# Kernel tuning notes

Hardware: AMD Instinct MI355X
Metric: run time of the kernel (lower is better)

Reference implementation:

```python
import jax, jax.numpy as jnp
import numpy as np

DIM, NH, NL, NP, HD, FF = 256, 8, 4, 4, 32, 1024
LN_EPS = 1e-5


def _ln(x, w, b):
    m = jnp.mean(x, axis=-1, keepdims=True)
    v = jnp.mean((x - m) ** 2, axis=-1, keepdims=True)
    return (x - m) * jax.lax.rsqrt(v + LN_EPS) * w + b


def _sample_level(value_l, loc, H, W):
    # value_l: (B, H*W, nH, hd) ; loc: (B, Lq, nH, P, 2) normalized coords in [0,1]
    B, Lq, nH, P, _ = loc.shape
    # grid_sample(align_corners=False): pixel coord = norm * size - 0.5
    x = loc[..., 0] * W - 0.5
    y = loc[..., 1] * H - 0.5
    x0 = jnp.floor(x)
    y0 = jnp.floor(y)
    wx1 = x - x0
    wy1 = y - y0
    wx0 = 1.0 - wx1
    wy0 = 1.0 - wy1
    x0i = x0.astype(jnp.int32)
    y0i = y0.astype(jnp.int32)

    def corner(xi, yi, w):
        valid = ((xi >= 0) & (xi < W) & (yi >= 0) & (yi < H)).astype(value_l.dtype)
        idx = jnp.clip(yi, 0, H - 1) * W + jnp.clip(xi, 0, W - 1)
        idx = idx.transpose(0, 1, 3, 2).reshape(B, Lq * P, nH, 1)  # per-head gather index
        v = jnp.take_along_axis(value_l, idx, axis=1).reshape(B, Lq, P, nH, -1)
        wm = (w * valid).transpose(0, 1, 3, 2)[..., None]  # (B,Lq,P,nH,1)
        return v * wm

    return (corner(x0i, y0i, wx0 * wy0) + corner(x0i + 1, y0i, wx1 * wy0)
            + corner(x0i, y0i + 1, wx0 * wy1) + corner(x0i + 1, y0i + 1, wx1 * wy1))


def _msdeform_attn(q, value, ref, shapes_np, starts_np, W_off, b_off, W_attn, b_attn):
    B, S, _ = q.shape
    off = (q @ W_off + b_off).reshape(B, S, NH, NL, NP, 2)
    attn = jax.nn.softmax((q @ W_attn + b_attn).reshape(B, S, NH, NL * NP), axis=-1)
    attn = attn.reshape(B, S, NH, NL, NP)
    # offset normalizer is (W, H) per level
    norm = jnp.asarray(shapes_np[:, ::-1].copy(), dtype=q.dtype)  # (NL, 2)
    loc = ref[:, :, None, :, None, :] + off / norm[None, None, None, :, None, :]
    outs = []
    for l in range(NL):
        H, W = int(shapes_np[l, 0]), int(shapes_np[l, 1])
        s = int(starts_np[l])
        vl = value[:, s:s + H * W]  # (B, H*W, NH, HD)
        outs.append(_sample_level(vl, loc[:, :, :, l], H, W))  # (B,S,P,NH,HD)
    samp = jnp.stack(outs, axis=2)  # (B,S,NL,P,NH,HD)
    w = attn.transpose(0, 1, 3, 4, 2)[..., None]  # (B,S,NL,P,NH,1)
    return (samp * w).sum(axis=(2, 3)).reshape(B, S, NH * HD)


def setup_inputs() -> dict:
    key = jax.random.key(0)
    ks = jax.random.split(key, 16)
    shapes = np.array([[64, 64], [32, 32], [16, 16], [8, 8]], dtype=np.int64)
    starts = np.array([0, 4096, 5120, 5376], dtype=np.int64)
    B, S = 4, 5440
    std = 0.02
    return {
        "input": jax.random.normal(ks[0], (B, S, DIM), jnp.float32),
        "pos": jax.random.normal(ks[1], (B, S, DIM), jnp.float32),
        "reference_point": jax.random.uniform(ks[2], (B, S, NL, 2), jnp.float32),
        "shape": shapes,
        "level_start": starts,
        "ln1_w": jnp.ones((DIM,), jnp.float32),
        "ln1_b": jnp.zeros((DIM,), jnp.float32),
        "W_off": jax.random.normal(ks[3], (DIM, NH * NL * NP * 2), jnp.float32) * std,
        "b_off": jax.random.normal(ks[4], (NH * NL * NP * 2,), jnp.float32) * 0.1,
        "W_attn": jax.random.normal(ks[5], (DIM, NH * NL * NP), jnp.float32) * std,
        "b_attn": jnp.zeros((NH * NL * NP,), jnp.float32),
        "W_val": jax.random.normal(ks[6], (DIM, DIM), jnp.float32) * std,
        "b_val": jnp.zeros((DIM,), jnp.float32),
        "W_out": jax.random.normal(ks[7], (DIM, DIM), jnp.float32) * std,
        "b_out": jnp.zeros((DIM,), jnp.float32),
        "ln2_w": jnp.ones((DIM,), jnp.float32),
        "ln2_b": jnp.zeros((DIM,), jnp.float32),
        "ff_w1": jax.random.normal(ks[8], (DIM, FF), jnp.float32) * std,
        "ff_b1": jnp.zeros((FF,), jnp.float32),
        "ff_w2": jax.random.normal(ks[9], (FF, DIM), jnp.float32) * std,
        "ff_b2": jnp.zeros((DIM,), jnp.float32),
    }


def reference(input, pos, reference_point, shape, level_start,
              ln1_w, ln1_b, W_off, b_off, W_attn, b_attn, W_val, b_val,
              W_out, b_out, ln2_w, ln2_b, ff_w1, ff_b1, ff_w2, ff_b2):
    shapes_np = np.asarray(shape)
    starts_np = np.asarray(level_start)
    B, S, _ = input.shape
    # pre-norm query with positional embedding
    q = _ln(input, ln1_w, ln1_b) + pos
    # value projection acts on the raw residual stream (input_flatten)
    value = (input @ W_val + b_val).reshape(B, S, NH, HD)
    attn_out = _msdeform_attn(q, value, reference_point, shapes_np, starts_np,
                              W_off, b_off, W_attn, b_attn) @ W_out + b_out
    x = input + attn_out  # dropout is identity in eval
    y = _ln(x, ln2_w, ln2_b)
    ff = jax.nn.relu(y @ ff_w1 + ff_b1) @ ff_w2 + ff_b2
    return x + ff
```

## Files before the change

### kernel.cpp

```cpp
#include <hip/hip_runtime.h>
#include <math.h>

#define DIM 256
#define NHEAD 8
#define NLVL 4
#define NPT 4
#define HDIM 32
#define FFDIM 1024
#define BATCH 4
#define SEQ 5440
#define MTOK (BATCH * SEQ)

typedef __attribute__((ext_vector_type(8))) short short8;
typedef __attribute__((ext_vector_type(4))) float f32x4;

__device__ __forceinline__ unsigned short f2bf(float f) {
    union { float f; unsigned int u; } x; x.f = f;
    unsigned int r = x.u + 0x7fffu + ((x.u >> 16) & 1u);
    return (unsigned short)(r >> 16);
}
__device__ __forceinline__ float bf_lo(unsigned int u) {
    union { unsigned int u; float f; } x; x.u = u << 16;
    return x.f;
}
__device__ __forceinline__ float bf_hi(unsigned int u) {
    union { unsigned int u; float f; } x; x.u = u & 0xffff0000u;
    return x.f;
}

__global__ __launch_bounds__(256) void wtprep_kernel(
    const float* __restrict__ W_val, const float* __restrict__ W_off,
    const float* __restrict__ W_attn, const float* __restrict__ W_out,
    const float* __restrict__ ff_w1, const float* __restrict__ ff_w2,
    unsigned short* __restrict__ wts)
{
    int idx = blockIdx.x * 256 + threadIdx.x;
    const float* W; int K, N, base;
    if      (idx < 65536)  { W = W_val;  K = 256;  N = 256;  base = 0; }
    else if (idx < 131072) { W = W_off;  K = 256;  N = 256;  base = 65536; }
    else if (idx < 163840) { W = W_attn; K = 256;  N = 128;  base = 131072; }
    else if (idx < 229376) { W = W_out;  K = 256;  N = 256;  base = 163840; }
    else if (idx < 491520) { W = ff_w1;  K = 256;  N = 1024; base = 229376; }
    else if (idx < 753664) { W = ff_w2;  K = 1024; N = 256;  base = 491520; }
    else return;
    int li = idx - base;
    int k = li % K;
    int n = li / K;
    wts[idx] = f2bf(W[(size_t)k * N + n]);
}

template<int COPY_BF16>
__global__ __launch_bounds__(256) void ln_kernel(
    const float* __restrict__ x, const float* __restrict__ w,
    const float* __restrict__ bvec, const float* __restrict__ addend,
    unsigned short* __restrict__ out, unsigned short* __restrict__ xbf)
{
    int wv = threadIdx.x >> 6, lane = threadIdx.x & 63;
    int token = blockIdx.x * 4 + wv;
    size_t base = (size_t)token * DIM + lane * 4;
    float4 v = *(const float4*)(x + base);
    float s  = v.x + v.y + v.z + v.w;
    float s2 = v.x * v.x + v.y * v.y + v.z * v.z + v.w * v.w;
    #pragma unroll
    for (int o = 1; o < 64; o <<= 1) {
        s  += __shfl_xor(s, o);
        s2 += __shfl_xor(s2, o);
    }
    float m  = s * (1.0f / DIM);
    float rs = rsqrtf(s2 * (1.0f / DIM) - m * m + 1e-5f);
    float4 w4 = *(const float4*)(w + lane * 4);
    float4 b4 = *(const float4*)(bvec + lane * 4);
    float4 r;
    r.x = (v.x - m) * rs * w4.x + b4.x;
    r.y = (v.y - m) * rs * w4.y + b4.y;
    r.z = (v.z - m) * rs * w4.z + b4.z;
    r.w = (v.w - m) * rs * w4.w + b4.w;
    if (addend) {
        float4 a = *(const float4*)(addend + base);
        r.x += a.x; r.y += a.y; r.z += a.z; r.w += a.w;
    }
    ushort4 o4;
    o4.x = f2bf(r.x); o4.y = f2bf(r.y); o4.z = f2bf(r.z); o4.w = f2bf(r.w);
    *(ushort4*)(out + base) = o4;
    if (COPY_BF16) {
        ushort4 c;
        c.x = f2bf(v.x); c.y = f2bf(v.y); c.z = f2bf(v.z); c.w = f2bf(v.w);
        *(ushort4*)(xbf + base) = c;
    }
}

#define LDSTR 40

template<int OUT_BF16, int RELU, int HAS_RES>
__global__ __launch_bounds__(256) void mfma_gemm(
    const unsigned short* __restrict__ A,
    const unsigned short* __restrict__ Bt,
    const float* __restrict__ bias,
    const float* __restrict__ res,
    void* __restrict__ Cout,
    int M, int N, int K)
{
    __shared__ __align__(16) unsigned short As[128 * LDSTR];
    __shared__ __align__(16) unsigned short Bs[128 * LDSTR];

    const int tid  = threadIdx.x;
    const int lane = tid & 63;
    const int wv   = tid >> 6;
    const int wr   = wv >> 1;
    const int wc   = wv & 1;
    const int m16  = lane & 15;
    const int quad = lane >> 4;

    const int bm0 = blockIdx.y * 128;
    const int bn0 = blockIdx.x * 128;

    const int srow = tid >> 2;
    const int scol = (tid & 3) * 8;

    f32x4 acc[4][4] = {};

    for (int k0 = 0; k0 < K; k0 += 32) {
        uint4 av0 = *(const uint4*)(A  + (size_t)(bm0 + srow)      * K + k0 + scol);
        uint4 av1 = *(const uint4*)(A  + (size_t)(bm0 + srow + 64) * K + k0 + scol);
        uint4 bv0 = *(const uint4*)(Bt + (size_t)(bn0 + srow)      * K + k0 + scol);
        uint4 bv1 = *(const uint4*)(Bt + (size_t)(bn0 + srow + 64) * K + k0 + scol);
        if (k0) __syncthreads();
        *(uint4*)&As[(srow)      * LDSTR + scol] = av0;
        *(uint4*)&As[(srow + 64) * LDSTR + scol] = av1;
        *(uint4*)&Bs[(srow)      * LDSTR + scol] = bv0;
        *(uint4*)&Bs[(srow + 64) * LDSTR + scol] = bv1;
        __syncthreads();

        short8 af[4], bf[4];
        #pragma unroll
        for (int i = 0; i < 4; i++)
            af[i] = *(const short8*)&As[(wr * 64 + i * 16 + m16) * LDSTR + quad * 8];
        #pragma unroll
        for (int j = 0; j < 4; j++)
            bf[j] = *(const short8*)&Bs[(wc * 64 + j * 16 + m16) * LDSTR + quad * 8];

        #pragma unroll
        for (int i = 0; i < 4; i++)
            #pragma unroll
            for (int j = 0; j < 4; j++)
                acc[i][j] = __builtin_amdgcn_mfma_f32_16x16x32_bf16(
                    af[i], bf[j], acc[i][j], 0, 0, 0);
    }

    #pragma unroll
    for (int i = 0; i < 4; i++) {
        #pragma unroll
        for (int j = 0; j < 4; j++) {
            int colb = bn0 + wc * 64 + j * 16 + m16;
            float bcol = bias[colb];
            #pragma unroll
            for (int r = 0; r < 4; r++) {
                int rowb = bm0 + wr * 64 + i * 16 + quad * 4 + r;
                float v = acc[i][j][r] + bcol;
                if (HAS_RES) v += res[(size_t)rowb * N + colb];
                if (RELU) v = fmaxf(v, 0.0f);
                if (OUT_BF16)
                    ((unsigned short*)Cout)[(size_t)rowb * N + colb] = f2bf(v);
                else
                    ((float*)Cout)[(size_t)rowb * N + colb] = v;
            }
        }
    }
}

__global__ __launch_bounds__(256) void msdeform_kernel(
    const unsigned short* __restrict__ value,
    const float* __restrict__ off_buf,
    const float* __restrict__ attn_buf,
    const float* __restrict__ ref,
    unsigned short* __restrict__ samp_out)
{
    const int Hs[NLVL] = {64, 32, 16, 8};
    const int Ws[NLVL] = {64, 32, 16, 8};
    const int St[NLVL] = {0, 4096, 5120, 5376};

    const int t  = threadIdx.x;
    const int tt = t >> 5;
    const int h  = (t >> 2) & 7;
    const int dg = t & 3;
    const int token = blockIdx.x * 8 + tt;
    const int b = token / SEQ;

    __shared__ float s_attn[8][NHEAD][16];
    __shared__ float s_loc[8][NHEAD][16][2];

    float4 a4 = *(const float4*)(attn_buf + (size_t)token * 128 + h * 16 + dg * 4);
    *(float4*)&s_attn[tt][h][dg * 4] = a4;

    const float* offp = off_buf + (size_t)token * 256 + h * 32 + dg * 8;
    float4 o0 = *(const float4*)(offp);
    float4 o1 = *(const float4*)(offp + 4);
    float fWd = (float)Ws[dg], fHd = (float)Hs[dg];
    float rx = ref[(size_t)token * 8 + dg * 2 + 0];
    float ry = ref[(size_t)token * 8 + dg * 2 + 1];
    s_loc[tt][h][dg * 4 + 0][0] = rx + o0.x / fWd;
    s_loc[tt][h][dg * 4 + 0][1] = ry + o0.y / fHd;
    s_loc[tt][h][dg * 4 + 1][0] = rx + o0.z / fWd;
    s_loc[tt][h][dg * 4 + 1][1] = ry + o0.w / fHd;
    s_loc[tt][h][dg * 4 + 2][0] = rx + o1.x / fWd;
    s_loc[tt][h][dg * 4 + 2][1] = ry + o1.y / fHd;
    s_loc[tt][h][dg * 4 + 3][0] = rx + o1.z / fWd;
    s_loc[tt][h][dg * 4 + 3][1] = ry + o1.w / fHd;
    __syncthreads();

    if (dg == 0) {
        float mx = -1e30f;
        #pragma unroll
        for (int i = 0; i < 16; i++) mx = fmaxf(mx, s_attn[tt][h][i]);
        float sum = 0.0f;
        #pragma unroll
        for (int i = 0; i < 16; i++) {
            float e = __expf(s_attn[tt][h][i] - mx);
            s_attn[tt][h][i] = e;
            sum += e;
        }
        float inv = 1.0f / sum;
        #pragma unroll
        for (int i = 0; i < 16; i++) s_attn[tt][h][i] *= inv;
    }
    __syncthreads();

    const size_t vbase = ((size_t)b * SEQ) * DIM + h * HDIM + dg * 8;

    float acc[8] = {};
    #pragma unroll
    for (int l = 0; l < NLVL; l++) {
        const int Hl = Hs[l], Wl = Ws[l], s0 = St[l];
        const float fW = (float)Wl, fH = (float)Hl;
        #pragma unroll
        for (int p = 0; p < NPT; p++) {
            int i = l * 4 + p;
            float aw = s_attn[tt][h][i];
            float x = s_loc[tt][h][i][0] * fW - 0.5f;
            float y = s_loc[tt][h][i][1] * fH - 0.5f;
            float x0f = floorf(x), y0f = floorf(y);
            float wx1 = x - x0f, wy1 = y - y0f;
            float wx0 = 1.0f - wx1, wy0 = 1.0f - wy1;
            int x0 = (int)x0f, y0 = (int)y0f;
            #pragma unroll
            for (int cy = 0; cy < 2; cy++) {
                int yi = y0 + cy;
                bool vy = (yi >= 0) && (yi < Hl);
                int yc = min(max(yi, 0), Hl - 1);
                float wy = cy ? wy1 : wy0;
                #pragma unroll
                for (int cx = 0; cx < 2; cx++) {
                    int xi = x0 + cx;
                    bool vx = (xi >= 0) && (xi < Wl);
                    int xc = min(max(xi, 0), Wl - 1);
                    float cw = aw * wy * (cx ? wx1 : wx0) * ((vx && vy) ? 1.0f : 0.0f);
                    uint4 v = *(const uint4*)(value + vbase + (size_t)(s0 + yc * Wl + xc) * DIM);
                    acc[0] = fmaf(cw, bf_lo(v.x), acc[0]);
                    acc[1] = fmaf(cw, bf_hi(v.x), acc[1]);
                    acc[2] = fmaf(cw, bf_lo(v.y), acc[2]);
                    acc[3] = fmaf(cw, bf_hi(v.y), acc[3]);
                    acc[4] = fmaf(cw, bf_lo(v.z), acc[4]);
                    acc[5] = fmaf(cw, bf_hi(v.z), acc[5]);
                    acc[6] = fmaf(cw, bf_lo(v.w), acc[6]);
                    acc[7] = fmaf(cw, bf_hi(v.w), acc[7]);
                }
            }
        }
    }

    uint4 o;
    o.x = (unsigned int)f2bf(acc[0]) | ((unsigned int)f2bf(acc[1]) << 16);
    o.y = (unsigned int)f2bf(acc[2]) | ((unsigned int)f2bf(acc[3]) << 16);
    o.z = (unsigned int)f2bf(acc[4]) | ((unsigned int)f2bf(acc[5]) << 16);
    o.w = (unsigned int)f2bf(acc[6]) | ((unsigned int)f2bf(acc[7]) << 16);
    *(uint4*)(samp_out + (size_t)token * DIM + h * HDIM + dg * 8) = o;
}

extern "C" void kernel_launch(void* const* d_in, const int* in_sizes, int n_in,
                              void* d_out, int out_size, void* d_ws, size_t ws_size,
                              hipStream_t stream) {
    const float* input = (const float*)d_in[0];
    const float* pos   = (const float*)d_in[1];
    const float* ref   = (const float*)d_in[2];
    const float* ln1_w = (const float*)d_in[5];
    const float* ln1_b = (const float*)d_in[6];
    const float* W_off = (const float*)d_in[7];
    const float* b_off = (const float*)d_in[8];
    const float* W_attn = (const float*)d_in[9];
    const float* b_attn = (const float*)d_in[10];
    const float* W_val = (const float*)d_in[11];
    const float* b_val = (const float*)d_in[12];
    const float* W_out = (const float*)d_in[13];
    const float* b_out = (const float*)d_in[14];
    const float* ln2_w = (const float*)d_in[15];
    const float* ln2_b = (const float*)d_in[16];
    const float* ff_w1 = (const float*)d_in[17];
    const float* ff_b1 = (const float*)d_in[18];
    const float* ff_w2 = (const float*)d_in[19];
    const float* ff_b2 = (const float*)d_in[20];
    float* out = (float*)d_out;

    const size_t M = MTOK;
    float* ws = (float*)d_ws;

    unsigned short* input_bf = (unsigned short*)(ws);
    unsigned short* y_bf     = input_bf;
    unsigned short* q_bf     = (unsigned short*)(ws + M * 128);
    unsigned short* samp_bf  = q_bf;
    float*  off_buf  = ws + M * 256;
    float*  x_buf    = off_buf;
    float*  attn_buf = ws + M * 512;
    unsigned short* val_bf   = (unsigned short*)(ws + M * 640);
    unsigned short* h_bf     = (unsigned short*)(ws + M * 512);
    unsigned short* wts      = (unsigned short*)(ws + M * 1024);

    unsigned short* wval_t  = wts;
    unsigned short* woff_t  = wval_t  + 256 * 256;
    unsigned short* wattn_t = woff_t  + 256 * 256;
    unsigned short* wout_t  = wattn_t + 128 * 256;
    unsigned short* ffw1_t  = wout_t  + 256 * 256;
    unsigned short* ffw2_t  = ffw1_t  + 1024 * 256;

    dim3 blk(256);

    wtprep_kernel<<<dim3((753664 + 255) / 256), blk, 0, stream>>>(
        W_val, W_off, W_attn, W_out, ff_w1, ff_w2, wts);

    ln_kernel<1><<<dim3(M / 4), blk, 0, stream>>>(
        input, ln1_w, ln1_b, pos, q_bf, input_bf);

    mfma_gemm<1,0,0><<<dim3(256/128, M/128), blk, 0, stream>>>(
        input_bf, wval_t, b_val, nullptr, val_bf, M, 256, 256);

    mfma_gemm<0,0,0><<<dim3(256/128, M/128), blk, 0, stream>>>(
        q_bf, woff_t, b_off, nullptr, off_buf, M, 256, 256);

    mfma_gemm<0,0,0><<<dim3(128/128, M/128), blk, 0, stream>>>(
        q_bf, wattn_t, b_attn, nullptr, attn_buf, M, 128, 256);

    msdeform_kernel<<<dim3(M / 8), blk, 0, stream>>>(
        val_bf, off_buf, attn_buf, ref, samp_bf);

    mfma_gemm<0,0,1><<<dim3(256/128, M/128), blk, 0, stream>>>(
        samp_bf, wout_t, b_out, input, x_buf, M, 256, 256);

    ln_kernel<0><<<dim3(M / 4), blk, 0, stream>>>(
        x_buf, ln2_w, ln2_b, nullptr, y_bf, nullptr);

    mfma_gemm<1,1,0><<<dim3(1024/128, M/128), blk, 0, stream>>>(
        y_bf, ffw1_t, ff_b1, nullptr, h_bf, M, 1024, 256);

    mfma_gemm<0,0,1><<<dim3(256/128, M/128), blk, 0, stream>>>(
        h_bf, ffw2_t, ff_b2, x_buf, out, M, 256, 1024);
}
```

Before: 308.1 us.

## Fuse offset/attn GEMMs, use direct-to-LDS loads, fp16 value sampling with precomputed tables

The offset and attention-logit projections are merged into a single N=384 GEMM with a combined bias, which removes one launch and one re-read of the query. The GEMM now stages tiles with global_load_lds straight into unpadded LDS, fixes K at compile time, and swaps the MFMA operand order so the epilogue writes float4/ushort4 vectors. The value projection is written in fp16. The deformable sampling kernel gives each thread one level, builds a shared table of corner offsets and fp16 weights, then gathers with packed half2 FMAs. The fp16 value storage and half-precision accumulation may lower accuracy, and the unpadded LDS layout may cause bank conflicts.

```diff
diff --git a/kernel.cpp b/kernel.cpp
--- a/kernel.cpp
+++ b/kernel.cpp
@@ -1,4 +1,5 @@
 #include <hip/hip_runtime.h>
+#include <hip/hip_fp16.h>
 #include <math.h>
 
 #define DIM 256
@@ -19,22 +20,26 @@
     unsigned int r = x.u + 0x7fffu + ((x.u >> 16) & 1u);
     return (unsigned short)(r >> 16);
 }
-__device__ __forceinline__ float bf_lo(unsigned int u) {
-    union { unsigned int u; float f; } x; x.u = u << 16;
-    return x.f;
-}
-__device__ __forceinline__ float bf_hi(unsigned int u) {
-    union { unsigned int u; float f; } x; x.u = u & 0xffff0000u;
-    return x.f;
+
+__device__ __forceinline__ void gll16(const unsigned short* g, unsigned short* l) {
+    __builtin_amdgcn_global_load_lds(
+        (const __attribute__((address_space(1))) void*)g,
+        (__attribute__((address_space(3))) void*)l,
+        16, 0, 0);
 }
 
 __global__ __launch_bounds__(256) void wtprep_kernel(
     const float* __restrict__ W_val, const float* __restrict__ W_off,
     const float* __restrict__ W_attn, const float* __restrict__ W_out,
     const float* __restrict__ ff_w1, const float* __restrict__ ff_w2,
-    unsigned short* __restrict__ wts)
+    const float* __restrict__ b_off, const float* __restrict__ b_attn,
+    unsigned short* __restrict__ wts, float* __restrict__ bcomb)
 {
     int idx = blockIdx.x * 256 + threadIdx.x;
+    if (blockIdx.x == 0 && threadIdx.x < 384) {
+        int li = threadIdx.x;
+        bcomb[li] = (li < 256) ? b_off[li] : b_attn[li - 256];
+    }
     const float* W; int K, N, base;
     if      (idx < 65536)  { W = W_val;  K = 256;  N = 256;  base = 0; }
     else if (idx < 131072) { W = W_off;  K = 256;  N = 256;  base = 65536; }
@@ -89,19 +94,17 @@
     }
 }
 
-#define LDSTR 40
-
-template<int OUT_BF16, int RELU, int HAS_RES>
+template<int K, int OUT, int RELU, int HAS_RES>
 __global__ __launch_bounds__(256) void mfma_gemm(
     const unsigned short* __restrict__ A,
     const unsigned short* __restrict__ Bt,
     const float* __restrict__ bias,
     const float* __restrict__ res,
     void* __restrict__ Cout,
-    int M, int N, int K)
+    int M, int N)
 {
-    __shared__ __align__(16) unsigned short As[128 * LDSTR];
-    __shared__ __align__(16) unsigned short Bs[128 * LDSTR];
+    __shared__ __align__(16) unsigned short As[128 * 32];
+    __shared__ __align__(16) unsigned short Bs[128 * 32];
 
     const int tid  = threadIdx.x;
     const int lane = tid & 63;
@@ -114,64 +117,82 @@
     const int bm0 = blockIdx.y * 128;
     const int bn0 = blockIdx.x * 128;
 
-    const int srow = tid >> 2;
-    const int scol = (tid & 3) * 8;
+    const int e0 = wv * 1024 + lane * 8;
+    const int e1 = e0 + 512;
+    const int r0 = e0 >> 5, c0 = e0 & 31;
+    const int r1 = e1 >> 5, c1 = e1 & 31;
 
     f32x4 acc[4][4] = {};
 
     for (int k0 = 0; k0 < K; k0 += 32) {
-        uint4 av0 = *(const uint4*)(A  + (size_t)(bm0 + srow)      * K + k0 + scol);
-        uint4 av1 = *(const uint4*)(A  + (size_t)(bm0 + srow + 64) * K + k0 + scol);
-        uint4 bv0 = *(const uint4*)(Bt + (size_t)(bn0 + srow)      * K + k0 + scol);
-        uint4 bv1 = *(const uint4*)(Bt + (size_t)(bn0 + srow + 64) * K + k0 + scol);
         if (k0) __syncthreads();
-        *(uint4*)&As[(srow)      * LDSTR + scol] = av0;
-        *(uint4*)&As[(srow + 64) * LDSTR + scol] = av1;
-        *(uint4*)&Bs[(srow)      * LDSTR + scol] = bv0;
-        *(uint4*)&Bs[(srow + 64) * LDSTR + scol] = bv1;
+        gll16(A  + (size_t)(bm0 + r0) * K + k0 + c0, As + e0);
+        gll16(A  + (size_t)(bm0 + r1) * K + k0 + c1, As + e1);
+        gll16(Bt + (size_t)(bn0 + r0) * K + k0 + c0, Bs + e0);
+        gll16(Bt + (size_t)(bn0 + r1) * K + k0 + c1, Bs + e1);
         __syncthreads();
 
         short8 af[4], bf[4];
         #pragma unroll
         for (int i = 0; i < 4; i++)
-            af[i] = *(const short8*)&As[(wr * 64 + i * 16 + m16) * LDSTR + quad * 8];
+            af[i] = *(const short8*)&As[(wr * 64 + i * 16 + m16) * 32 + quad * 8];
         #pragma unroll
         for (int j = 0; j < 4; j++)
-            bf[j] = *(const short8*)&Bs[(wc * 64 + j * 16 + m16) * LDSTR + quad * 8];
+            bf[j] = *(const short8*)&Bs[(wc * 64 + j * 16 + m16) * 32 + quad * 8];
 
         #pragma unroll
         for (int i = 0; i < 4; i++)
             #pragma unroll
             for (int j = 0; j < 4; j++)
                 acc[i][j] = __builtin_amdgcn_mfma_f32_16x16x32_bf16(
-                    af[i], bf[j], acc[i][j], 0, 0, 0);
-    }
+                    bf[j], af[i], acc[i][j], 0, 0, 0);
+    }
+
+    float4 bias4[4];
+    #pragma unroll
+    for (int j = 0; j < 4; j++)
+        bias4[j] = *(const float4*)(bias + bn0 + wc * 64 + j * 16 + quad * 4);
 
     #pragma unroll
     for (int i = 0; i < 4; i++) {
+        int row = bm0 + wr * 64 + i * 16 + m16;
         #pragma unroll
         for (int j = 0; j < 4; j++) {
-            int colb = bn0 + wc * 64 + j * 16 + m16;
-            float bcol = bias[colb];
-            #pragma unroll
-            for (int r = 0; r < 4; r++) {
-                int rowb = bm0 + wr * 64 + i * 16 + quad * 4 + r;
-                float v = acc[i][j][r] + bcol;
-                if (HAS_RES) v += res[(size_t)rowb * N + colb];
-                if (RELU) v = fmaxf(v, 0.0f);
-                if (OUT_BF16)
-                    ((unsigned short*)Cout)[(size_t)rowb * N + colb] = f2bf(v);
-                else
-                    ((float*)Cout)[(size_t)rowb * N + colb] = v;
+            int col = bn0 + wc * 64 + j * 16 + quad * 4;
+            float v0 = acc[i][j][0] + bias4[j].x;
+            float v1 = acc[i][j][1] + bias4[j].y;
+            float v2 = acc[i][j][2] + bias4[j].z;
+            float v3 = acc[i][j][3] + bias4[j].w;
+            if (HAS_RES) {
+                float4 rr = *(const float4*)(res + (size_t)row * N + col);
+                v0 += rr.x; v1 += rr.y; v2 += rr.z; v3 += rr.w;
+            }
+            if (RELU) {
+                v0 = fmaxf(v0, 0.0f); v1 = fmaxf(v1, 0.0f);
+                v2 = fmaxf(v2, 0.0f); v3 = fmaxf(v3, 0.0f);
+            }
+            if (OUT == 0) {
+                float4 o = {v0, v1, v2, v3};
+                *(float4*)((float*)Cout + (size_t)row * N + col) = o;
+            } else if (OUT == 1) {
+                ushort4 o;
+                o.x = f2bf(v0); o.y = f2bf(v1); o.z = f2bf(v2); o.w = f2bf(v3);
+                *(ushort4*)((unsigned short*)Cout + (size_t)row * N + col) = o;
+            } else {
+                ushort4 o;
+                o.x = __half_as_ushort(__float2half_rn(v0));
+                o.y = __half_as_ushort(__float2half_rn(v1));
+                o.z = __half_as_ushort(__float2half_rn(v2));
+                o.w = __half_as_ushort(__float2half_rn(v3));
+                *(ushort4*)((unsigned short*)Cout + (size_t)row * N + col) = o;
             }
         }
     }
 }
 
 __global__ __launch_bounds__(256) void msdeform_kernel(
-    const unsigned short* __restrict__ value,
-    const float* __restrict__ off_buf,
-    const float* __restrict__ attn_buf,
+    const unsigned short* __restrict__ value_h,
+    const float* __restrict__ oa,
     const float* __restrict__ ref,
     unsigned short* __restrict__ samp_out)
 {
@@ -181,63 +202,44 @@
 
     const int t  = threadIdx.x;
     const int tt = t >> 5;
-    const int h  = (t >> 2) & 7;
-    const int dg = t & 3;
+    const int rr = t & 31;
+    const int h  = rr >> 2;
+    const int q  = rr & 3;
     const int token = blockIdx.x * 8 + tt;
     const int b = token / SEQ;
 
-    __shared__ float s_attn[8][NHEAD][16];
-    __shared__ float s_loc[8][NHEAD][16][2];
-
-    float4 a4 = *(const float4*)(attn_buf + (size_t)token * 128 + h * 16 + dg * 4);
-    *(float4*)&s_attn[tt][h][dg * 4] = a4;
-
-    const float* offp = off_buf + (size_t)token * 256 + h * 32 + dg * 8;
-    float4 o0 = *(const float4*)(offp);
-    float4 o1 = *(const float4*)(offp + 4);
-    float fWd = (float)Ws[dg], fHd = (float)Hs[dg];
-    float rx = ref[(size_t)token * 8 + dg * 2 + 0];
-    float ry = ref[(size_t)token * 8 + dg * 2 + 1];
-    s_loc[tt][h][dg * 4 + 0][0] = rx + o0.x / fWd;
-    s_loc[tt][h][dg * 4 + 0][1] = ry + o0.y / fHd;
-    s_loc[tt][h][dg * 4 + 1][0] = rx + o0.z / fWd;
-    s_loc[tt][h][dg * 4 + 1][1] = ry + o0.w / fHd;
-    s_loc[tt][h][dg * 4 + 2][0] = rx + o1.x / fWd;
-    s_loc[tt][h][dg * 4 + 2][1] = ry + o1.y / fHd;
-    s_loc[tt][h][dg * 4 + 3][0] = rx + o1.z / fWd;
-    s_loc[tt][h][dg * 4 + 3][1] = ry + o1.w / fHd;
+    __shared__ float s_attn[8][8][17];
+    __shared__ uint2 s_tab[8][8][65];
+
+    const float* oat = oa + (size_t)token * 384;
+    float4 a4 = *(const float4*)(oat + 256 + h * 16 + q * 4);
+    s_attn[tt][h][q * 4 + 0] = a4.x;
+    s_attn[tt][h][q * 4 + 1] = a4.y;
+    s_attn[tt][h][q * 4 + 2] = a4.z;
+    s_attn[tt][h][q * 4 + 3] = a4.w;
+    float4 o0 = *(const float4*)(oat + h * 32 + q * 8);
+    float4 o1 = *(const float4*)(oat + h * 32 + q * 8 + 4);
+    float2 rf = *(const float2*)(ref + (size_t)token * 8 + q * 2);
     __syncthreads();
 
-    if (dg == 0) {
-        float mx = -1e30f;
-        #pragma unroll
-        for (int i = 0; i < 16; i++) mx = fmaxf(mx, s_attn[tt][h][i]);
-        float sum = 0.0f;
-        #pragma unroll
-        for (int i = 0; i < 16; i++) {
-            float e = __expf(s_attn[tt][h][i] - mx);
-            s_attn[tt][h][i] = e;
-            sum += e;
-        }
-        float inv = 1.0f / sum;
-        #pragma unroll
-        for (int i = 0; i < 16; i++) s_attn[tt][h][i] *= inv;
-    }
-    __syncthreads();
-
-    const size_t vbase = ((size_t)b * SEQ) * DIM + h * HDIM + dg * 8;
-
-    float acc[8] = {};
-    #pragma unroll
-    for (int l = 0; l < NLVL; l++) {
-        const int Hl = Hs[l], Wl = Ws[l], s0 = St[l];
+    float mx = -1e30f;
+    #pragma unroll
+    for (int i = 0; i < 16; i++) mx = fmaxf(mx, s_attn[tt][h][i]);
+    float sum = 0.0f;
+    #pragma unroll
+    for (int i = 0; i < 16; i++) sum += __expf(s_attn[tt][h][i] - mx);
+    float inv = 1.0f / sum;
+
+    {
+        const int Hl = Hs[q], Wl = Ws[q], s0 = St[q];
         const float fW = (float)Wl, fH = (float)Hl;
         #pragma unroll
-        for (int p = 0; p < NPT; p++) {
-            int i = l * 4 + p;
-            float aw = s_attn[tt][h][i];
-            float x = s_loc[tt][h][i][0] * fW - 0.5f;
-            float y = s_loc[tt][h][i][1] * fH - 0.5f;
+        for (int p = 0; p < 4; p++) {
+            float ox = (p == 0) ? o0.x : (p == 1) ? o0.z : (p == 2) ? o1.x : o1.z;
+            float oy = (p == 0) ? o0.y : (p == 1) ? o0.w : (p == 2) ? o1.y : o1.w;
+            float aw = __expf(s_attn[tt][h][q * 4 + p] - mx) * inv;
+            float x = (rf.x + ox / fW) * fW - 0.5f;
+            float y = (rf.y + oy / fH) * fH - 0.5f;
             float x0f = floorf(x), y0f = floorf(y);
             float wx1 = x - x0f, wy1 = y - y0f;
             float wx0 = 1.0f - wx1, wy0 = 1.0f - wy1;
@@ -253,27 +255,42 @@
                     int xi = x0 + cx;
                     bool vx = (xi >= 0) && (xi < Wl);
                     int xc = min(max(xi, 0), Wl - 1);
-                    float cw = aw * wy * (cx ? wx1 : wx0) * ((vx && vy) ? 1.0f : 0.0f);
-                    uint4 v = *(const uint4*)(value + vbase + (size_t)(s0 + yc * Wl + xc) * DIM);
-                    acc[0] = fmaf(cw, bf_lo(v.x), acc[0]);
-                    acc[1] = fmaf(cw, bf_hi(v.x), acc[1]);
-                    acc[2] = fmaf(cw, bf_lo(v.y), acc[2]);
-                    acc[3] = fmaf(cw, bf_hi(v.y), acc[3]);
-                    acc[4] = fmaf(cw, bf_lo(v.z), acc[4]);
-                    acc[5] = fmaf(cw, bf_hi(v.z), acc[5]);
-                    acc[6] = fmaf(cw, bf_lo(v.w), acc[6]);
-                    acc[7] = fmaf(cw, bf_hi(v.w), acc[7]);
+                    float w = aw * wy * (cx ? wx1 : wx0) * ((vx && vy) ? 1.0f : 0.0f);
+                    unsigned int off = (unsigned int)(s0 + yc * Wl + xc) * 512u;
+                    unsigned short hw = __half_as_ushort(__float2half_rn(w));
+                    unsigned int wp = (unsigned int)hw | ((unsigned int)hw << 16);
+                    s_tab[tt][h][(q * 4 + p) * 4 + cy * 2 + cx] = make_uint2(off, wp);
                 }
             }
         }
     }
+    __syncthreads();
+
+    const char* vb = (const char*)value_h;
+    unsigned int cbase = (unsigned int)(b * (SEQ * 512)) + h * 64 + q * 16;
+    const uint2* tab = &s_tab[tt][h][0];
+
+    __half2 z; { union { unsigned int u; __half2 h; } c; c.u = 0; z = c.h; }
+    __half2 acc0 = z, acc1 = z, acc2 = z, acc3 = z;
+
+    #pragma unroll 16
+    for (int i = 0; i < 64; i++) {
+        uint2 e = tab[i];
+        uint4 v = *(const uint4*)(vb + (cbase + e.x));
+        union { unsigned int u; __half2 h; } wu; wu.u = e.y;
+        union { uint4 u; __half2 h[4]; } vu; vu.u = v;
+        acc0 = __hfma2(vu.h[0], wu.h, acc0);
+        acc1 = __hfma2(vu.h[1], wu.h, acc1);
+        acc2 = __hfma2(vu.h[2], wu.h, acc2);
+        acc3 = __hfma2(vu.h[3], wu.h, acc3);
+    }
 
     uint4 o;
-    o.x = (unsigned int)f2bf(acc[0]) | ((unsigned int)f2bf(acc[1]) << 16);
-    o.y = (unsigned int)f2bf(acc[2]) | ((unsigned int)f2bf(acc[3]) << 16);
-    o.z = (unsigned int)f2bf(acc[4]) | ((unsigned int)f2bf(acc[5]) << 16);
-    o.w = (unsigned int)f2bf(acc[6]) | ((unsigned int)f2bf(acc[7]) << 16);
-    *(uint4*)(samp_out + (size_t)token * DIM + h * HDIM + dg * 8) = o;
+    o.x = (unsigned int)f2bf(__low2float(acc0)) | ((unsigned int)f2bf(__high2float(acc0)) << 16);
+    o.y = (unsigned int)f2bf(__low2float(acc1)) | ((unsigned int)f2bf(__high2float(acc1)) << 16);
+    o.z = (unsigned int)f2bf(__low2float(acc2)) | ((unsigned int)f2bf(__high2float(acc2)) << 16);
+    o.w = (unsigned int)f2bf(__low2float(acc3)) | ((unsigned int)f2bf(__high2float(acc3)) << 16);
+    *(uint4*)(samp_out + (size_t)token * 256 + h * 32 + q * 8) = o;
 }
 
 extern "C" void kernel_launch(void* const* d_in, const int* in_sizes, int n_in,
@@ -307,49 +324,45 @@
     unsigned short* y_bf     = input_bf;
     unsigned short* q_bf     = (unsigned short*)(ws + M * 128);
     unsigned short* samp_bf  = q_bf;
-    float*  off_buf  = ws + M * 256;
-    float*  x_buf    = off_buf;
-    float*  attn_buf = ws + M * 512;
-    unsigned short* val_bf   = (unsigned short*)(ws + M * 640);
-    unsigned short* h_bf     = (unsigned short*)(ws + M * 512);
-    unsigned short* wts      = (unsigned short*)(ws + M * 1024);
+    float*  oa_buf   = ws + M * 256;
+    float*  x_buf    = oa_buf;
+    unsigned short* val_h = (unsigned short*)(ws + M * 640);
+    unsigned short* h_bf  = (unsigned short*)(ws + M * 768);
+    unsigned short* wts   = (unsigned short*)(ws + M * 1280);
+    float* bcomb = (float*)(wts + 753664);
 
     unsigned short* wval_t  = wts;
     unsigned short* woff_t  = wval_t  + 256 * 256;
-    unsigned short* wattn_t = woff_t  + 256 * 256;
-    unsigned short* wout_t  = wattn_t + 128 * 256;
+    unsigned short* wout_t  = woff_t  + 384 * 256;
     unsigned short* ffw1_t  = wout_t  + 256 * 256;
     unsigned short* ffw2_t  = ffw1_t  + 1024 * 256;
 
     dim3 blk(256);
 
-    wtprep_kernel<<<dim3((753664 + 255) / 256), blk, 0, stream>>>(
-        W_val, W_off, W_attn, W_out, ff_w1, ff_w2, wts);
+    wtprep_kernel<<<dim3(2944), blk, 0, stream>>>(
+        W_val, W_off, W_attn, W_out, ff_w1, ff_w2, b_off, b_attn, wts, bcomb);
 
     ln_kernel<1><<<dim3(M / 4), blk, 0, stream>>>(
         input, ln1_w, ln1_b, pos, q_bf, input_bf);
 
-    mfma_gemm<1,0,0><<<dim3(256/128, M/128), blk, 0, stream>>>(
-        input_bf, wval_t, b_val, nullptr, val_bf, M, 256, 256);
-
-    mfma_gemm<0,0,0><<<dim3(256/128, M/128), blk, 0, stream>>>(
-        q_bf, woff_t, b_off, nullptr, off_buf, M, 256, 256);
-
-    mfma_gemm<0,0,0><<<dim3(128/128, M/128), blk, 0, stream>>>(
-        q_bf, wattn_t, b_attn, nullptr, attn_buf, M, 128, 256);
+    mfma_gemm<256, 2, 0, 0><<<dim3(2, M / 128), blk, 0, stream>>>(
+        input_bf, wval_t, b_val, nullptr, val_h, M, 256);
+
+    mfma_gemm<256, 0, 0, 0><<<dim3(3, M / 128), blk, 0, stream>>>(
+        q_bf, woff_t, bcomb, nullptr, oa_buf, M, 384);
 
     msdeform_kernel<<<dim3(M / 8), blk, 0, stream>>>(
-        val_bf, off_buf, attn_buf, ref, samp_bf);
-
-    mfma_gemm<0,0,1><<<dim3(256/128, M/128), blk, 0, stream>>>(
-        samp_bf, wout_t, b_out, input, x_buf, M, 256, 256);
+        val_h, oa_buf, ref, samp_bf);
+
+    mfma_gemm<256, 0, 0, 1><<<dim3(2, M / 128), blk, 0, stream>>>(
+        samp_bf, wout_t, b_out, input, x_buf, M, 256);
 
     ln_kernel<0><<<dim3(M / 4), blk, 0, stream>>>(
         x_buf, ln2_w, ln2_b, nullptr, y_bf, nullptr);
 
-    mfma_gemm<1,1,0><<<dim3(1024/128, M/128), blk, 0, stream>>>(
-        y_bf, ffw1_t, ff_b1, nullptr, h_bf, M, 1024, 256);
-
-    mfma_gemm<0,0,1><<<dim3(256/128, M/128), blk, 0, stream>>>(
-        h_bf, ffw2_t, ff_b2, x_buf, out, M, 256, 1024);
-}
+    mfma_gemm<256, 1, 1, 0><<<dim3(8, M / 128), blk, 0, stream>>>(
+        y_bf, ffw1_t, ff_b1, nullptr, h_bf, M, 1024);
+
+    mfma_gemm<1024, 0, 0, 1><<<dim3(2, M / 128), blk, 0, stream>>>(
+        h_bf, ffw2_t, ff_b2, x_buf, out, M, 256);
+}
```

Result: faster. 269.7 us (-12.5%).
